# Optimization experiments

Hardware: AMD Instinct MI355X
Metric: run time of the kernel (lower is better)

## Reference

```python
import jax, jax.numpy as jnp
import numpy as np

WS = 7          # window size
NH = 6          # heads
LN_EPS = 1e-5


def _rel_pos_index(ws):
    coords = np.stack(np.meshgrid(np.arange(ws), np.arange(ws), indexing='ij'))  # (2, ws, ws)
    flat = coords.reshape(2, -1)                       # (2, ws*ws)
    rel = flat[:, :, None] - flat[:, None, :]          # (2, N, N)
    rel = rel.transpose(1, 2, 0).copy()
    rel[:, :, 0] += ws - 1
    rel[:, :, 1] += ws - 1
    rel[:, :, 0] *= 2 * ws - 1
    return jnp.asarray(rel.sum(-1).reshape(-1), dtype=jnp.int32)  # (N*N,)


def _layernorm(x, gamma, beta):
    mu = jnp.mean(x, axis=-1, keepdims=True)
    var = jnp.var(x, axis=-1, keepdims=True)
    return (x - mu) * jax.lax.rsqrt(var + LN_EPS) * gamma + beta


def _window_partition(x, ws):
    B, H, W, C = x.shape
    x = x.reshape(B, H // ws, ws, W // ws, ws, C)
    return x.transpose(0, 1, 3, 2, 4, 5).reshape(-1, ws * ws, C)


def _window_reverse(w, ws, H, W, B):
    C = w.shape[-1]
    x = w.reshape(B, H // ws, W // ws, ws, ws, C)
    return x.transpose(0, 1, 3, 2, 4, 5).reshape(B, H, W, C)


def setup_inputs() -> dict:
    key = jax.random.key(0)
    B, H, W, C = 32, 56, 56, 384
    N, hidden = H * W, 1536
    ks = jax.random.split(key, 9)
    s = 0.02
    return {
        'x':      jax.random.normal(ks[0], (B, N, C), jnp.float32),
        'gamma1': jnp.ones((C,), jnp.float32),
        'beta1':  jnp.zeros((C,), jnp.float32),
        'w_qkv':  jax.random.normal(ks[1], (C, 3 * C), jnp.float32) * s,
        'w_proj': jax.random.normal(ks[2], (C, C), jnp.float32) * s,
        'b_proj': jnp.zeros((C,), jnp.float32),
        'rel_bias': jax.random.normal(ks[3], ((2 * WS - 1) ** 2, NH), jnp.float32) * s,
        'gamma2': jnp.ones((C,), jnp.float32),
        'beta2':  jnp.zeros((C,), jnp.float32),
        'w_fc1':  jax.random.normal(ks[4], (C, hidden), jnp.float32) * s,
        'b_fc1':  jnp.zeros((hidden,), jnp.float32),
        'w_dw':   jax.random.normal(ks[5], (hidden, 1, 3, 3), jnp.float32) * s,
        'b_dw':   jnp.zeros((hidden,), jnp.float32),
        'w_fc2':  jax.random.normal(ks[6], (hidden, C), jnp.float32) * s,
        'b_fc2':  jnp.zeros((C,), jnp.float32),
        'H': H,
        'W': W,
    }


def reference(x, gamma1, beta1, w_qkv, w_proj, b_proj, rel_bias,
              gamma2, beta2, w_fc1, b_fc1, w_dw, b_dw, w_fc2, b_fc2, H, W):
    B, N, C = x.shape
    Nw = WS * WS
    hd = C // NH
    scale = hd ** -0.5

    # ---- window attention branch ----
    shortcut = x
    xn = _layernorm(x, gamma1, beta1)
    xw = _window_partition(xn.reshape(B, H, W, C), WS)      # (Bw, Nw, C)
    Bw = xw.shape[0]
    qkv = (xw @ w_qkv).reshape(Bw, Nw, 3, NH, hd)
    q, k, v = [qkv[:, :, i].transpose(0, 2, 1, 3) for i in range(3)]  # (Bw, NH, Nw, hd)
    attn = jnp.einsum('bhnd,bhmd->bhnm', q, k) * scale
    bias = rel_bias[_rel_pos_index(WS)].reshape(Nw, Nw, NH).transpose(2, 0, 1)
    attn = jax.nn.softmax(attn + bias[None], axis=-1)
    out = jnp.einsum('bhnm,bhmd->bhnd', attn, v).transpose(0, 2, 1, 3).reshape(Bw, Nw, C)
    out = out @ w_proj + b_proj
    x = shortcut + _window_reverse(out, WS, H, W, B).reshape(B, N, C)

    # ---- ConvFFN branch ----
    y = _layernorm(x, gamma2, beta2)
    y = y @ w_fc1 + b_fc1                                    # (B, N, hidden)
    hdim = y.shape[-1]
    y2 = y.transpose(0, 2, 1).reshape(B, hdim, H, W)         # NCHW
    y2 = jax.lax.conv_general_dilated(
        y2, w_dw, window_strides=(1, 1), padding='SAME',
        dimension_numbers=('NCHW', 'OIHW', 'NCHW'),
        feature_group_count=hdim) + b_dw[None, :, None, None]
    y = y2.reshape(B, hdim, N).transpose(0, 2, 1)
    y = jax.nn.gelu(y, approximate=False)
    y = y @ w_fc2 + b_fc2
    return x + y
```

## Files before the change

### kernel.cpp

```cpp
#include <hip/hip_runtime.h>
#include <math.h>


typedef __bf16 bf16x8 __attribute__((ext_vector_type(8)));
typedef float f32x4 __attribute__((ext_vector_type(4)));
typedef unsigned short u16x8 __attribute__((ext_vector_type(8)));

__device__ __forceinline__ float b2f(unsigned short u) {
    union { unsigned int i; float f; } x;
    x.i = ((unsigned int)u) << 16;
    return x.f;
}
__device__ __forceinline__ unsigned short f2b(float f) {
    union { float f; unsigned int i; } x;
    x.f = f;
    unsigned int i = x.i;
    return (unsigned short)((i + 0x7fffu + ((i >> 16) & 1u)) >> 16);
}
__device__ __forceinline__ float rd2(const float* pf, const unsigned short* pb,
                                     long i, int f32) {
    return f32 ? pf[i] : b2f(pb[i]);
}

__global__ void detect_dtype(const unsigned int* __restrict__ gamma1,
                             int* __restrict__ flag)
{
    if (threadIdx.x == 0) flag[0] = (gamma1[0] == 0x3F800000u) ? 1 : 0;
}

__global__ __launch_bounds__(256) void convert_smalls(
    const int* __restrict__ flag,
    const void* g1, const void* b1, const void* bp, const void* g2,
    const void* b2, const void* bf1, const void* wdw, const void* bdw,
    const void* bf2, const void* rb, unsigned short* __restrict__ dst)
{
    int i = blockIdx.x * 256 + threadIdx.x;
    if (i >= 20214) return;
    const int f = flag[0];
    const void* src; long j; int o = i;
    if      (i < 384)   { src = g1;  j = i; }
    else if (i < 768)   { src = b1;  j = i - 384; }
    else if (i < 1152)  { src = bp;  j = i - 768; }
    else if (i < 1536)  { src = g2;  j = i - 1152; }
    else if (i < 1920)  { src = b2;  j = i - 1536; }
    else if (i < 3456)  { src = bf1; j = i - 1920; }
    else if (i < 17280) {
        int d = i - 3456, k = d / 1536, ch = d % 1536;
        src = wdw; j = (long)ch * 9 + k;
    }
    else if (i < 18816) { src = bdw; j = i - 17280; }
    else if (i < 19200) { src = bf2; j = i - 18816; }
    else                { src = rb;  j = i - 19200; }
    float v = f ? ((const float*)src)[j] : b2f(((const unsigned short*)src)[j]);
    dst[o] = f2b(v);
}

__global__ __launch_bounds__(256) void transpose_any(
    const void* __restrict__ in, unsigned short* __restrict__ out,
    int R, int C, const int* __restrict__ flag)
{
    __shared__ unsigned short tile[32][33];
    const int f = flag[0];
    int tx = threadIdx.x & 31, ty = threadIdx.x >> 5;
    int rb = blockIdx.y * 32, cb = blockIdx.x * 32;
#pragma unroll
    for (int i = 0; i < 32; i += 8) {
        int r = rb + ty + i, c = cb + tx;
        if (r < R && c < C)
            tile[ty + i][tx] = f2b(rd2((const float*)in,
                                       (const unsigned short*)in,
                                       (long)r * C + c, f));
    }
    __syncthreads();
#pragma unroll
    for (int i = 0; i < 32; i += 8) {
        int c = cb + ty + i, r = rb + tx;
        if (c < C && r < R) out[(long)c * R + r] = tile[tx][ty + i];
    }
}

__global__ __launch_bounds__(256) void ln_kernel(
    const float* __restrict__ xf, const unsigned short* __restrict__ xb,
    const unsigned short* __restrict__ gamma,
    const unsigned short* __restrict__ beta,
    unsigned short* __restrict__ yout, int T,
    const int* __restrict__ flagp, int force_f32)
{
    int w = blockIdx.x * 4 + (threadIdx.x >> 6);
    int lane = threadIdx.x & 63;
    if (w >= T) return;
    const int f32 = force_f32 ? 1 : flagp[0];
    long base = (long)w * 384;
    float v[6];
    float s = 0.f;
#pragma unroll
    for (int i = 0; i < 6; ++i) {
        v[i] = rd2(xf, xb, base + lane + i * 64, f32);
        s += v[i];
    }
#pragma unroll
    for (int o = 32; o > 0; o >>= 1) s += __shfl_xor(s, o);
    float mu = s * (1.f / 384.f);
    float q = 0.f;
#pragma unroll
    for (int i = 0; i < 6; ++i) { float d = v[i] - mu; q += d * d; }
#pragma unroll
    for (int o = 32; o > 0; o >>= 1) q += __shfl_xor(q, o);
    float rs = rsqrtf(q * (1.f / 384.f) + 1e-5f);
#pragma unroll
    for (int i = 0; i < 6; ++i) {
        int cc = lane + i * 64;
        yout[base + cc] = f2b((v[i] - mu) * rs * b2f(gamma[cc]) + b2f(beta[cc]));
    }
}

template<int EPI, bool OUT_F32_S, bool RES_F32_S>
__global__ __launch_bounds__(256) void gemm_nt(
    const unsigned short* __restrict__ A,
    const unsigned short* __restrict__ BT,
    float* __restrict__ Cf, unsigned short* __restrict__ Cb,
    const unsigned short* __restrict__ bias,
    const float* __restrict__ Rf, const unsigned short* __restrict__ Rb,
    int M, int N, int K,
    const int* __restrict__ rflagp, const int* __restrict__ oflagp)
{
    __shared__ __align__(16) unsigned short ldsA[2][128 * 32];
    __shared__ __align__(16) unsigned short ldsB[2][128 * 32];
    const int tid = threadIdx.x;
    const int lane = tid & 63;
    const int wv = tid >> 6;
    const int waveM = wv >> 1, waveN = wv & 1;
    const long m0 = (long)blockIdx.x * 128;
    const long n0 = (long)blockIdx.y * 128;

    f32x4 acc[4][4] = {};

    const int c0 = tid, c1 = 256 + tid;
    const int r0 = c0 >> 2, q0 = (c0 & 3) ^ (r0 & 3);
    const int r1 = c1 >> 2, q1 = (c1 & 3) ^ (r1 & 3);
    long am0 = m0 + r0; if (am0 >= M) am0 = M - 1;
    long am1 = m0 + r1; if (am1 >= M) am1 = M - 1;
    const unsigned short* a0p = A + am0 * (long)K + q0 * 8;
    const unsigned short* a1p = A + am1 * (long)K + q1 * 8;
    const unsigned short* b0p = BT + (n0 + r0) * (long)K + q0 * 8;
    const unsigned short* b1p = BT + (n0 + r1) * (long)K + q1 * 8;

    const int rq = lane & 15, quad = lane >> 4;
    const int nt = K >> 5;

    auto STAGE = [&](int buf, int kt) {
        __builtin_amdgcn_global_load_lds(
            (const __attribute__((address_space(1))) void*)(a0p + kt),
            (__attribute__((address_space(3))) void*)(&ldsA[buf][c0 * 8]), 16, 0, 0);
        __builtin_amdgcn_global_load_lds(
            (const __attribute__((address_space(1))) void*)(a1p + kt),
            (__attribute__((address_space(3))) void*)(&ldsA[buf][c1 * 8]), 16, 0, 0);
        __builtin_amdgcn_global_load_lds(
            (const __attribute__((address_space(1))) void*)(b0p + kt),
            (__attribute__((address_space(3))) void*)(&ldsB[buf][c0 * 8]), 16, 0, 0);
        __builtin_amdgcn_global_load_lds(
            (const __attribute__((address_space(1))) void*)(b1p + kt),
            (__attribute__((address_space(3))) void*)(&ldsB[buf][c1 * 8]), 16, 0, 0);
    };

    STAGE(0, 0);
    __syncthreads();

    for (int t = 0; t < nt; ++t) {
        const int cur = t & 1;
        if (t + 1 < nt) STAGE(cur ^ 1, (t + 1) * 32);

        bf16x8 af[4], bfv[4];
#pragma unroll
        for (int mi = 0; mi < 4; ++mi) {
            int R = waveM * 64 + mi * 16 + rq;
            int ch = R * 4 + (quad ^ (R & 3));
            af[mi] = *(const bf16x8*)(&ldsA[cur][ch * 8]);
        }
#pragma unroll
        for (int ni = 0; ni < 4; ++ni) {
            int R = waveN * 64 + ni * 16 + rq;
            int ch = R * 4 + (quad ^ (R & 3));
            bfv[ni] = *(const bf16x8*)(&ldsB[cur][ch * 8]);
        }
#pragma unroll
        for (int mi = 0; mi < 4; ++mi)
#pragma unroll
            for (int ni = 0; ni < 4; ++ni)
                acc[mi][ni] = __builtin_amdgcn_mfma_f32_16x16x32_bf16(
                    af[mi], bfv[ni], acc[mi][ni], 0, 0, 0);

        __syncthreads();
    }

    const int res_f32 = rflagp ? rflagp[0] : (RES_F32_S ? 1 : 0);
    const int out_f32 = oflagp ? oflagp[0] : (OUT_F32_S ? 1 : 0);

    const int rq4 = (lane >> 4) * 4;
    const int coln = lane & 15;
#pragma unroll
    for (int mi = 0; mi < 4; ++mi) {
#pragma unroll
        for (int ni = 0; ni < 4; ++ni) {
            long col = n0 + waveN * 64 + ni * 16 + coln;
            float bv = (EPI >= 1) ? b2f(bias[col]) : 0.f;
#pragma unroll
            for (int r = 0; r < 4; ++r) {
                long row = m0 + waveM * 64 + mi * 16 + rq4 + r;
                if (row >= M) continue;
                long off = row * (long)N + col;
                float v = acc[mi][ni][r] + bv;
                if (EPI == 2) v += rd2(Rf, Rb, off, res_f32);
                if (out_f32) Cf[off] = v;
                else Cb[off] = f2b(v);
            }
        }
    }
}

__global__ __launch_bounds__(64) void attn_kernel(
    const unsigned short* __restrict__ qkv,
    const unsigned short* __restrict__ rel_bias,
    unsigned short* __restrict__ out)
{
    __shared__ __align__(16) unsigned short k_lds[64 * 72];
    __shared__ __align__(16) unsigned short v_lds[64 * 72];
    __shared__ __align__(16) unsigned short q_lds[64 * 72];

    const int w = blockIdx.x, hh = blockIdx.y;
    const int lane = threadIdx.x;
    const int b = w >> 6, wh = (w >> 3) & 7, ww = w & 7;
    const long base = (long)b * 3136;
    const unsigned short* src = qkv + hh * 64;

#pragma unroll
    for (int it = 0; it < 13; ++it) {
        int idx = it * 64 + lane;
        if (idx < 784) {
            int t = idx >> 4, d4 = (idx & 15) << 2;
            int pi = t / 7, pj = t % 7;
            const unsigned short* gp =
                src + (base + (wh * 7 + pi) * 56 + (ww * 7 + pj)) * 1152 + d4;
            *(ushort4*)(q_lds + t * 72 + d4) = *(const ushort4*)(gp);
            *(ushort4*)(k_lds + t * 72 + d4) = *(const ushort4*)(gp + 384);
        }
    }
    for (int p = 0; p < 49; ++p) {
        int pi = p / 7, pj = p % 7;
        v_lds[lane * 72 + p] =
            src[(base + (wh * 7 + pi) * 56 + (ww * 7 + pj)) * 1152 + 768 + lane];
    }
#pragma unroll
    for (int p = 49; p < 64; ++p) v_lds[lane * 72 + p] = 0;
    __syncthreads();

    const int rq = lane & 15, quad = lane >> 4;

    bf16x8 kf[4][2], qf[4][2];
#pragma unroll
    for (int t4 = 0; t4 < 4; ++t4)
#pragma unroll
        for (int ks = 0; ks < 2; ++ks) {
            kf[t4][ks] = *(const bf16x8*)(k_lds + (t4 * 16 + rq) * 72 + ks * 32 + quad * 8);
            qf[t4][ks] = *(const bf16x8*)(q_lds + (t4 * 16 + rq) * 72 + ks * 32 + quad * 8);
        }
    f32x4 sa[4][4] = {};
#pragma unroll
    for (int ks = 0; ks < 2; ++ks)
#pragma unroll
        for (int mi = 0; mi < 4; ++mi)
#pragma unroll
            for (int ni = 0; ni < 4; ++ni)
                sa[mi][ni] = __builtin_amdgcn_mfma_f32_16x16x32_bf16(
                    kf[mi][ks], qf[ni][ks], sa[mi][ni], 0, 0, 0);

    const int kq = quad * 4;
#pragma unroll
    for (int ni = 0; ni < 4; ++ni) {
        int q = ni * 16 + rq;
        int qc = (q < 49) ? q : 48;
        int yi = qc / 7, xi = qc % 7;
        float mx = -1e30f;
#pragma unroll
        for (int mi = 0; mi < 4; ++mi)
#pragma unroll
            for (int r = 0; r < 4; ++r) {
                int key = mi * 16 + kq + r;
                float s;
                if (key < 49) {
                    int yj = key / 7, xj = key % 7;
                    int idx = (yi - yj + 6) * 13 + (xi - xj + 6);
                    s = 0.125f * sa[mi][ni][r] + b2f(rel_bias[idx * 6 + hh]);
                } else s = -1e30f;
                sa[mi][ni][r] = s;
                mx = fmaxf(mx, s);
            }
        mx = fmaxf(mx, __shfl_xor(mx, 16));
        mx = fmaxf(mx, __shfl_xor(mx, 32));
        float sum = 0.f;
#pragma unroll
        for (int mi = 0; mi < 4; ++mi)
#pragma unroll
            for (int r = 0; r < 4; ++r) {
                float e = __expf(sa[mi][ni][r] - mx);
                sa[mi][ni][r] = e;
                sum += e;
            }
        sum += __shfl_xor(sum, 16);
        sum += __shfl_xor(sum, 32);
        float rinv = 1.f / sum;
#pragma unroll
        for (int mi = 0; mi < 4; ++mi) {
            unsigned int w0 = (unsigned int)f2b(sa[mi][ni][0] * rinv) |
                              ((unsigned int)f2b(sa[mi][ni][1] * rinv) << 16);
            unsigned int w1 = (unsigned int)f2b(sa[mi][ni][2] * rinv) |
                              ((unsigned int)f2b(sa[mi][ni][3] * rinv) << 16);
            *(unsigned int*)(q_lds + q * 72 + mi * 16 + kq)     = w0;
            *(unsigned int*)(q_lds + q * 72 + mi * 16 + kq + 2) = w1;
        }
    }
    __syncthreads();

    f32x4 oa[4][4] = {};
#pragma unroll
    for (int ks = 0; ks < 2; ++ks) {
        bf16x8 pf[4], vf[4];
#pragma unroll
        for (int qt = 0; qt < 4; ++qt)
            pf[qt] = *(const bf16x8*)(q_lds + (qt * 16 + rq) * 72 + ks * 32 + quad * 8);
#pragma unroll
        for (int dt = 0; dt < 4; ++dt)
            vf[dt] = *(const bf16x8*)(v_lds + (dt * 16 + rq) * 72 + ks * 32 + quad * 8);
#pragma unroll
        for (int qt = 0; qt < 4; ++qt)
#pragma unroll
            for (int dt = 0; dt < 4; ++dt)
                oa[qt][dt] = __builtin_amdgcn_mfma_f32_16x16x32_bf16(
                    pf[qt], vf[dt], oa[qt][dt], 0, 0, 0);
    }

#pragma unroll
    for (int qt = 0; qt < 4; ++qt)
#pragma unroll
        for (int r = 0; r < 4; ++r) {
            int q = qt * 16 + quad * 4 + r;
            if (q >= 49) continue;
            int yi = q / 7, xi = q % 7;
            long t = base + (long)(wh * 7 + yi) * 56 + (ww * 7 + xi);
            unsigned short* op = out + t * 384 + hh * 64;
#pragma unroll
            for (int dt = 0; dt < 4; ++dt)
                op[dt * 16 + rq] = f2b(oa[qt][dt][r]);
        }
}

__global__ __launch_bounds__(192) void dwconv_gelu(
    const unsigned short* __restrict__ h,
    const unsigned short* __restrict__ w_dwT,
    const unsigned short* __restrict__ b_dw,
    unsigned short* __restrict__ g)
{
    const long t = blockIdx.x;
    const int bb = (int)(t / 3136), n = (int)(t % 3136);
    const int r = n / 56, c = n % 56;
    const int ch = threadIdx.x * 8;

    float a[8];
    u16x8 bv = *(const u16x8*)(b_dw + ch);
#pragma unroll
    for (int i = 0; i < 8; ++i) a[i] = b2f(bv[i]);

#pragma unroll
    for (int dr = -1; dr <= 1; ++dr) {
        int rr = r + dr;
        if (rr < 0 || rr >= 56) continue;
#pragma unroll
        for (int dc = -1; dc <= 1; ++dc) {
            int cc = c + dc;
            if (cc < 0 || cc >= 56) continue;
            int k = (dr + 1) * 3 + (dc + 1);
            long off = ((long)bb * 3136 + rr * 56 + cc) * 1536 + ch;
            u16x8 hv = *(const u16x8*)(h + off);
            u16x8 wv = *(const u16x8*)(w_dwT + k * 1536 + ch);
#pragma unroll
            for (int i = 0; i < 8; ++i) a[i] += b2f(hv[i]) * b2f(wv[i]);
        }
    }
    u16x8 ov;
#pragma unroll
    for (int i = 0; i < 8; ++i) {
        float v = 0.5f * a[i] * (1.f + erff(a[i] * 0.70710678118654752f));
        ov[i] = f2b(v);
    }
    *(u16x8*)(g + t * 1536 + ch) = ov;
}

extern "C" void kernel_launch(void* const* d_in, const int* in_sizes, int n_in,
                              void* d_out, int out_size, void* d_ws, size_t ws_size,
                              hipStream_t stream)
{
    const void* x      = d_in[0];
    const void* gamma1 = d_in[1];
    const void* beta1  = d_in[2];
    const void* w_qkv  = d_in[3];
    const void* w_proj = d_in[4];
    const void* b_proj = d_in[5];
    const void* relb   = d_in[6];
    const void* gamma2 = d_in[7];
    const void* beta2  = d_in[8];
    const void* w_fc1  = d_in[9];
    const void* b_fc1  = d_in[10];
    const void* w_dw   = d_in[11];
    const void* b_dw   = d_in[12];
    const void* w_fc2  = d_in[13];
    const void* b_fc2  = d_in[14];

    const int NIMG = 32, NPI = 3136;

    int* flag = (int*)d_ws;
    unsigned short* smalls = (unsigned short*)((char*)d_ws + 16);
    unsigned short* wqkvT  = (unsigned short*)((char*)d_ws + 16 + 20224 * 2);
    unsigned short* wprojT = wqkvT + 1152 * 384;
    unsigned short* wfc1T  = wprojT + 384 * 384;
    unsigned short* wfc2T  = wfc1T + 1536 * 384;
    const size_t WB = 16 + 20224 * 2 +
        ((size_t)1152 * 384 + 384 * 384 + 1536 * 384 + 384 * 1536) * 2;
    char* chunk_base = (char*)d_ws + WB;

    const unsigned short* c_g1   = smalls;
    const unsigned short* c_b1   = smalls + 384;
    const unsigned short* c_bp   = smalls + 768;
    const unsigned short* c_g2   = smalls + 1152;
    const unsigned short* c_b2   = smalls + 1536;
    const unsigned short* c_bf1  = smalls + 1920;
    const unsigned short* c_wdwT = smalls + 3456;
    const unsigned short* c_bdw  = smalls + 17280;
    const unsigned short* c_bf2  = smalls + 18816;
    const unsigned short* c_rb   = smalls + 19200;

    const size_t PER_IMG = (size_t)NPI * 384 * 4 + 2 * (size_t)NPI * 1536 * 2;
    int ipc = NIMG;
    while (ipc > 1 && WB + PER_IMG * (size_t)ipc > ws_size) ipc >>= 1;

    detect_dtype<<<1, 64, 0, stream>>>((const unsigned int*)gamma1, flag);
    convert_smalls<<<80, 256, 0, stream>>>(flag, gamma1, beta1, b_proj, gamma2,
        beta2, b_fc1, w_dw, b_dw, b_fc2, relb, smalls);
    transpose_any<<<dim3(36, 12), 256, 0, stream>>>(w_qkv, wqkvT, 384, 1152, flag);
    transpose_any<<<dim3(12, 12), 256, 0, stream>>>(w_proj, wprojT, 384, 384, flag);
    transpose_any<<<dim3(48, 12), 256, 0, stream>>>(w_fc1, wfc1T, 384, 1536, flag);
    transpose_any<<<dim3(12, 48), 256, 0, stream>>>(w_fc2, wfc2T, 1536, 384, flag);

    for (int i0 = 0; i0 < NIMG; i0 += ipc) {
        const int Tc = ipc * NPI;
        const long tb = (long)i0 * NPI;
        const int GM = (Tc + 127) / 128;

        float* x1 = (float*)chunk_base;
        unsigned short* r1 = (unsigned short*)(chunk_base + (size_t)Tc * 384 * 4);
        unsigned short* r2 = r1 + (size_t)Tc * 1536;

        unsigned short* xn      = r1;
        unsigned short* hbuf    = r1;
        unsigned short* qkv     = r2;
        unsigned short* attnout = r2 + (size_t)Tc * 1152;
        unsigned short* ybuf    = r2;
        unsigned short* gbuf    = r2;

        const float* xf = (const float*)x + tb * 384;
        const unsigned short* xb = (const unsigned short*)x + tb * 384;
        float* of = (float*)d_out + tb * 384;
        unsigned short* ob = (unsigned short*)d_out + tb * 384;

        ln_kernel<<<Tc / 4, 256, 0, stream>>>(xf, xb, c_g1, c_b1, xn, Tc, flag, 0);
        gemm_nt<0, false, false><<<dim3(GM, 9), 256, 0, stream>>>(
            xn, wqkvT, nullptr, qkv, nullptr, nullptr, nullptr,
            Tc, 1152, 384, nullptr, nullptr);
        attn_kernel<<<dim3(ipc * 64, 6), 64, 0, stream>>>(qkv, c_rb, attnout);
        gemm_nt<2, true, false><<<dim3(GM, 3), 256, 0, stream>>>(
            attnout, wprojT, x1, nullptr, c_bp, xf, xb,
            Tc, 384, 384, flag, nullptr);

        ln_kernel<<<Tc / 4, 256, 0, stream>>>(x1, nullptr, c_g2, c_b2, ybuf, Tc,
                                              flag, 1);
        gemm_nt<1, false, false><<<dim3(GM, 12), 256, 0, stream>>>(
            ybuf, wfc1T, nullptr, hbuf, c_bf1, nullptr, nullptr,
            Tc, 1536, 384, nullptr, nullptr);
        dwconv_gelu<<<Tc, 192, 0, stream>>>(hbuf, c_wdwT, c_bdw, gbuf);
        gemm_nt<2, false, true><<<dim3(GM, 3), 256, 0, stream>>>(
            gbuf, wfc2T, of, ob, c_bf2, x1, nullptr,
            Tc, 384, 1536, nullptr, flag);
    }
}
```

Measured before the change: 2.098 ms.

## Enlarge GEMM tile to 256x128 with 8 waves and deeper async LDS prefetch

The GEMM block grows from 256 to 512 threads and its M tile doubles to 256 rows, so each B tile loaded into LDS is shared by twice as many output rows. The staging loop now prefetches two k-tiles ahead, using explicit vmcnt waits and raw barriers instead of __syncthreads. The LDS swizzle also mixes more row bits to cut bank conflicts. In exchange, LDS use per block rises, the grid shrinks along M, and occupancy or tail balance may suffer.

```diff
diff --git a/kernel.cpp b/kernel.cpp
--- a/kernel.cpp
+++ b/kernel.cpp
@@ -20,6 +20,9 @@
 __device__ __forceinline__ float rd2(const float* pf, const unsigned short* pb,
                                      long i, int f32) {
     return f32 ? pf[i] : b2f(pb[i]);
+}
+__device__ __forceinline__ int xr_swz(int r) {
+    return (r & 3) ^ ((r >> 2) & 3);
 }
 
 __global__ void detect_dtype(const unsigned int* __restrict__ gamma1,
@@ -115,7 +118,7 @@
 }
 
 template<int EPI, bool OUT_F32_S, bool RES_F32_S>
-__global__ __launch_bounds__(256) void gemm_nt(
+__global__ __launch_bounds__(512) void gemm_nt(
     const unsigned short* __restrict__ A,
     const unsigned short* __restrict__ BT,
     float* __restrict__ Cf, unsigned short* __restrict__ Cb,
@@ -124,26 +127,26 @@
     int M, int N, int K,
     const int* __restrict__ rflagp, const int* __restrict__ oflagp)
 {
-    __shared__ __align__(16) unsigned short ldsA[2][128 * 32];
+    __shared__ __align__(16) unsigned short ldsA[2][256 * 32];
     __shared__ __align__(16) unsigned short ldsB[2][128 * 32];
     const int tid = threadIdx.x;
     const int lane = tid & 63;
     const int wv = tid >> 6;
     const int waveM = wv >> 1, waveN = wv & 1;
-    const long m0 = (long)blockIdx.x * 128;
+    const long m0 = (long)blockIdx.x * 256;
     const long n0 = (long)blockIdx.y * 128;
 
     f32x4 acc[4][4] = {};
 
-    const int c0 = tid, c1 = 256 + tid;
-    const int r0 = c0 >> 2, q0 = (c0 & 3) ^ (r0 & 3);
-    const int r1 = c1 >> 2, q1 = (c1 & 3) ^ (r1 & 3);
-    long am0 = m0 + r0; if (am0 >= M) am0 = M - 1;
-    long am1 = m0 + r1; if (am1 >= M) am1 = M - 1;
-    const unsigned short* a0p = A + am0 * (long)K + q0 * 8;
-    const unsigned short* a1p = A + am1 * (long)K + q1 * 8;
-    const unsigned short* b0p = BT + (n0 + r0) * (long)K + q0 * 8;
-    const unsigned short* b1p = BT + (n0 + r1) * (long)K + q1 * 8;
+    const int ca0 = tid, ca1 = 512 + tid, cb0 = tid;
+    const int ra0 = ca0 >> 2, qa0 = (ca0 & 3) ^ xr_swz(ra0);
+    const int ra1 = ca1 >> 2, qa1 = (ca1 & 3) ^ xr_swz(ra1);
+    const int rb0 = cb0 >> 2, qb0 = (cb0 & 3) ^ xr_swz(rb0);
+    long am0 = m0 + ra0; if (am0 >= M) am0 = M - 1;
+    long am1 = m0 + ra1; if (am1 >= M) am1 = M - 1;
+    const unsigned short* a0p = A + am0 * (long)K + qa0 * 8;
+    const unsigned short* a1p = A + am1 * (long)K + qa1 * 8;
+    const unsigned short* b0p = BT + (n0 + rb0) * (long)K + qb0 * 8;
 
     const int rq = lane & 15, quad = lane >> 4;
     const int nt = K >> 5;
@@ -151,36 +154,35 @@
     auto STAGE = [&](int buf, int kt) {
         __builtin_amdgcn_global_load_lds(
             (const __attribute__((address_space(1))) void*)(a0p + kt),
-            (__attribute__((address_space(3))) void*)(&ldsA[buf][c0 * 8]), 16, 0, 0);
+            (__attribute__((address_space(3))) void*)(&ldsA[buf][ca0 * 8]), 16, 0, 0);
         __builtin_amdgcn_global_load_lds(
             (const __attribute__((address_space(1))) void*)(a1p + kt),
-            (__attribute__((address_space(3))) void*)(&ldsA[buf][c1 * 8]), 16, 0, 0);
+            (__attribute__((address_space(3))) void*)(&ldsA[buf][ca1 * 8]), 16, 0, 0);
         __builtin_amdgcn_global_load_lds(
             (const __attribute__((address_space(1))) void*)(b0p + kt),
-            (__attribute__((address_space(3))) void*)(&ldsB[buf][c0 * 8]), 16, 0, 0);
-        __builtin_amdgcn_global_load_lds(
-            (const __attribute__((address_space(1))) void*)(b1p + kt),
-            (__attribute__((address_space(3))) void*)(&ldsB[buf][c1 * 8]), 16, 0, 0);
+            (__attribute__((address_space(3))) void*)(&ldsB[buf][cb0 * 8]), 16, 0, 0);
     };
 
     STAGE(0, 0);
-    __syncthreads();
+    if (nt > 1) STAGE(1, 32);
 
     for (int t = 0; t < nt; ++t) {
         const int cur = t & 1;
-        if (t + 1 < nt) STAGE(cur ^ 1, (t + 1) * 32);
+        if (t + 1 < nt) asm volatile("s_waitcnt vmcnt(3)" ::: "memory");
+        else            asm volatile("s_waitcnt vmcnt(0)" ::: "memory");
+        __builtin_amdgcn_s_barrier();
 
         bf16x8 af[4], bfv[4];
 #pragma unroll
         for (int mi = 0; mi < 4; ++mi) {
             int R = waveM * 64 + mi * 16 + rq;
-            int ch = R * 4 + (quad ^ (R & 3));
+            int ch = R * 4 + (quad ^ xr_swz(R));
             af[mi] = *(const bf16x8*)(&ldsA[cur][ch * 8]);
         }
 #pragma unroll
         for (int ni = 0; ni < 4; ++ni) {
             int R = waveN * 64 + ni * 16 + rq;
-            int ch = R * 4 + (quad ^ (R & 3));
+            int ch = R * 4 + (quad ^ xr_swz(R));
             bfv[ni] = *(const bf16x8*)(&ldsB[cur][ch * 8]);
         }
 #pragma unroll
@@ -190,7 +192,8 @@
                 acc[mi][ni] = __builtin_amdgcn_mfma_f32_16x16x32_bf16(
                     af[mi], bfv[ni], acc[mi][ni], 0, 0, 0);
 
-        __syncthreads();
+        __builtin_amdgcn_s_barrier();
+        if (t + 2 < nt) STAGE(cur, (t + 2) * 32);
     }
 
     const int res_f32 = rflagp ? rflagp[0] : (RES_F32_S ? 1 : 0);
@@ -453,7 +456,7 @@
     for (int i0 = 0; i0 < NIMG; i0 += ipc) {
         const int Tc = ipc * NPI;
         const long tb = (long)i0 * NPI;
-        const int GM = (Tc + 127) / 128;
+        const int GM = (Tc + 255) / 256;
 
         float* x1 = (float*)chunk_base;
         unsigned short* r1 = (unsigned short*)(chunk_base + (size_t)Tc * 384 * 4);
@@ -472,21 +475,21 @@
         unsigned short* ob = (unsigned short*)d_out + tb * 384;
 
         ln_kernel<<<Tc / 4, 256, 0, stream>>>(xf, xb, c_g1, c_b1, xn, Tc, flag, 0);
-        gemm_nt<0, false, false><<<dim3(GM, 9), 256, 0, stream>>>(
+        gemm_nt<0, false, false><<<dim3(GM, 9), 512, 0, stream>>>(
             xn, wqkvT, nullptr, qkv, nullptr, nullptr, nullptr,
             Tc, 1152, 384, nullptr, nullptr);
         attn_kernel<<<dim3(ipc * 64, 6), 64, 0, stream>>>(qkv, c_rb, attnout);
-        gemm_nt<2, true, false><<<dim3(GM, 3), 256, 0, stream>>>(
+        gemm_nt<2, true, false><<<dim3(GM, 3), 512, 0, stream>>>(
             attnout, wprojT, x1, nullptr, c_bp, xf, xb,
             Tc, 384, 384, flag, nullptr);
 
         ln_kernel<<<Tc / 4, 256, 0, stream>>>(x1, nullptr, c_g2, c_b2, ybuf, Tc,
                                               flag, 1);
-        gemm_nt<1, false, false><<<dim3(GM, 12), 256, 0, stream>>>(
+        gemm_nt<1, false, false><<<dim3(GM, 12), 512, 0, stream>>>(
             ybuf, wfc1T, nullptr, hbuf, c_bf1, nullptr, nullptr,
             Tc, 1536, 384, nullptr, nullptr);
         dwconv_gelu<<<Tc, 192, 0, stream>>>(hbuf, c_wdwT, c_bdw, gbuf);
-        gemm_nt<2, false, true><<<dim3(GM, 3), 256, 0, stream>>>(
+        gemm_nt<2, false, true><<<dim3(GM, 3), 512, 0, stream>>>(
             gbuf, wfc2T, of, ob, c_bf2, x1, nullptr,
             Tc, 384, 1536, nullptr, flag);
     }
```

New measurement: 2.128 ms. Within noise of the previous version (+1.4%).
